# Kernel optimization log

Hardware: AMD Instinct MI355X
Metric: run time of the kernel (lower is better)

The kernel has to match this reference:

```python
import jax, jax.numpy as jnp
import numpy as np

S, P = 64, 32          # scenes, pedestrians per scene (uniform)
N = S * P              # total pedestrians = 2048
H, E = 64, 64          # h_dim, embedding_dim
D1, D2 = 512, 1024     # mlp_pre_pool hidden, bottleneck_dim
EPS = 1e-5             # torch BatchNorm1d eps


def _batchnorm(x, gamma, beta):
    # Training-mode BN with per-scene batch stats (matches the per-scene
    # loop in the original, where BN sees one scene's num_ped^2 rows).
    # x: [S, P*P, D]
    mu = jnp.mean(x, axis=1, keepdims=True)
    var = jnp.mean(jnp.square(x - mu), axis=1, keepdims=True)  # biased var, as torch BN
    return (x - mu) * jax.lax.rsqrt(var + EPS) * gamma + beta


def setup_inputs() -> dict:
    key = jax.random.key(0)
    ks = jax.random.split(key, 16)
    h_states = jax.random.normal(ks[0], (1, N, H), jnp.float32)
    starts = jnp.arange(S, dtype=jnp.int32) * P
    seq_start_end = jnp.stack([starts, starts + P], axis=1)  # [S, 2]
    end_pos = jax.random.normal(ks[1], (N, 2), jnp.float32)
    rel_pos = jax.random.normal(ks[2], (N, 2), jnp.float32)  # unused (pooling_dim=2) but a fwd arg
    sc = 0.05
    params = dict(
        W_embed=jax.random.normal(ks[3], (2, E), jnp.float32) * sc,
        b_embed=jnp.zeros((E,), jnp.float32),
        W1=jax.random.normal(ks[4], (E + H, D1), jnp.float32) * sc,
        b1=jnp.zeros((D1,), jnp.float32),
        g1=jnp.ones((D1,), jnp.float32),
        be1=jnp.zeros((D1,), jnp.float32),
        W2=jax.random.normal(ks[5], (D1, D2), jnp.float32) * sc,
        b2=jnp.zeros((D2,), jnp.float32),
        g2=jnp.ones((D2,), jnp.float32),
        be2=jnp.zeros((D2,), jnp.float32),
    )
    return dict(h_states=h_states, seq_start_end=seq_start_end,
                end_pos=end_pos, rel_pos=rel_pos, **params)


def reference(h_states, seq_start_end, end_pos, rel_pos,
              W_embed, b_embed, W1, b1, g1, be1, W2, b2, g2, be2):
    # Uniform scenes: seq_start_end delimits S contiguous blocks of P peds.
    pos = end_pos.reshape(S, P, 2)
    h = h_states.reshape(N, H).reshape(S, P, H)
    # Original indexing: row (k*P + j) -> pos[j] - pos[k], hidden[j];
    # the final view(P, P, -1).max(1) maxes over j for each k.
    rel = pos[:, None, :, :] - pos[:, :, None, :]          # [S, Pk, Pj, 2]
    emb = rel @ W_embed + b_embed                          # [S, Pk, Pj, E]
    hid = jnp.broadcast_to(h[:, None, :, :], (S, P, P, H)) # hidden of j
    x = jnp.concatenate([emb, hid], axis=-1).reshape(S, P * P, E + H)
    x = jax.nn.relu(_batchnorm(x @ W1 + b1, g1, be1))      # [S, P*P, 512]
    x = jax.nn.relu(_batchnorm(x @ W2 + b2, g2, be2))      # [S, P*P, 1024]
    pool_h = x.reshape(S, P, P, D2).max(axis=2)            # max over j
    return pool_h.reshape(N, D2)
```

## Files before the change

### kernel.cpp

```cpp
#include <hip/hip_runtime.h>
#include <hip/hip_bf16.h>

#define S_ 64
#define P_ 32
#define N_ 2048
#define H_ 64
#define E_ 64
#define D1_ 512
#define D2_ 1024
#define EPS_ 1e-5f

typedef unsigned short u16;
using bf16x8 = __attribute__((ext_vector_type(8))) __bf16;
using floatx4 = __attribute__((ext_vector_type(4))) float;

__device__ inline u16 f2bf(float x) {
    unsigned u = __float_as_uint(x);
    unsigned r = (u + 0x7fffu + ((u >> 16) & 1u)) >> 16;
    return (u16)r;
}


__device__ void prep_scene_256(int u, int tid, float* smem,
                               const float* __restrict__ pos, const float* __restrict__ h,
                               const float* __restrict__ We, const float* __restrict__ W1,
                               const float* __restrict__ g1, const float* __restrict__ be1,
                               float* __restrict__ A, float* __restrict__ Bv) {
    const int s = u >> 2, dq = u & 3;
    const int jg = tid >> 7, dl = tid & 127;
    const int d = (dq << 7) + dl;
    float* hs = smem;
    float* ps = smem + 2048;
    float* red = smem + 2112;
    for (int i = tid; i < 2048; i += 256) hs[i] = h[(size_t)s * 2048 + i];
    if (tid < 64) ps[tid] = pos[s * 64 + tid];
    __syncthreads();
    float wq0 = 0.f, wq1 = 0.f;
    for (int e = 0; e < 64; ++e) {
        const float wv = W1[e * 512 + d];
        wq0 += We[e] * wv;
        wq1 += We[64 + e] * wv;
    }
    float w[16], uu[16];
#pragma unroll
    for (int jj = 0; jj < 16; ++jj) w[jj] = 0.f;
    const float4* h4 = (const float4*)hs;
    for (int e4 = 0; e4 < 16; ++e4) {
        const float c0 = W1[(64 + e4 * 4 + 0) * 512 + d];
        const float c1 = W1[(64 + e4 * 4 + 1) * 512 + d];
        const float c2 = W1[(64 + e4 * 4 + 2) * 512 + d];
        const float c3 = W1[(64 + e4 * 4 + 3) * 512 + d];
#pragma unroll
        for (int jj = 0; jj < 16; ++jj) {
            const float4 hv = h4[((jg << 4) + jj) * 16 + e4];
            w[jj] += hv.x * c0 + hv.y * c1 + hv.z * c2 + hv.w * c3;
        }
    }
    float sw = 0.f, sww = 0.f, su = 0.f, suu = 0.f;
#pragma unroll
    for (int jj = 0; jj < 16; ++jj) {
        const int j = (jg << 4) + jj;
        uu[jj] = ps[2 * j] * wq0 + ps[2 * j + 1] * wq1;
        w[jj] += uu[jj];
        sw += w[jj]; sww += w[jj] * w[jj];
        su += uu[jj]; suu += uu[jj] * uu[jj];
    }
    red[(jg << 7) + dl] = sw;
    red[256 + (jg << 7) + dl] = sww;
    red[512 + (jg << 7) + dl] = su;
    red[768 + (jg << 7) + dl] = suu;
    __syncthreads();
    const float tw = red[dl] + red[128 + dl];
    const float tww = red[256 + dl] + red[384 + dl];
    const float tu = red[512 + dl] + red[640 + dl];
    const float tuu = red[768 + dl] + red[896 + dl];
    const float mw = tw * (1.f / 32.f), mu2 = tu * (1.f / 32.f);
    const float var = (tww * (1.f / 32.f) - mw * mw) + (tuu * (1.f / 32.f) - mu2 * mu2);
    const float sc = rsqrtf(var + EPS_) * g1[d];
    const float bb = be1[d];
#pragma unroll
    for (int jj = 0; jj < 16; ++jj) {
        const int j = (jg << 4) + jj;
        A[(size_t)(s * 32 + j) * 512 + d] = (w[jj] - mw) * sc + bb;
        Bv[(size_t)(s * 32 + j) * 512 + d] = (uu[jj] - mu2) * sc;
    }
}

__device__ void w2t_tile_256(int b2, int tid, void* smem,
                             const float* __restrict__ W2, u16* __restrict__ w2t) {
    float (*tile)[65] = (float (*)[65])smem;
    const int bi = b2 & 15, bj = b2 >> 4;
    const int tx = tid & 63, ty = tid >> 6;
#pragma unroll
    for (int i = 0; i < 64; i += 4)
        tile[ty + i][tx] = W2[(size_t)(bj * 64 + ty + i) * 1024 + bi * 64 + tx];
    __syncthreads();
#pragma unroll
    for (int i = 0; i < 64; i += 4)
        w2t[(size_t)(bi * 64 + ty + i) * 512 + bj * 64 + tx] = f2bf(tile[tx][ty + i]);
}

__global__ __launch_bounds__(256, 2)
void k_gemm(const float* __restrict__ A, const float* __restrict__ Bv,
            const u16* __restrict__ w2t, const float* __restrict__ g2,
            float* __restrict__ ext,
            float* __restrict__ psum, float* __restrict__ psumsq) {
    __shared__ __align__(16) u16 As[128 * 64];
    __shared__ __align__(16) u16 Ws[256 * 64];
    const int tid = threadIdx.x;
    const int bid = blockIdx.x;
    if (bid & 1) {
        __builtin_amdgcn_s_sleep(27);
    }
    const int wave = tid >> 6, lane = tid & 63;
    const int wm = wave >> 1, wn = wave & 1;
    const int quad = lane >> 4, l16 = lane & 15;
    const int lrow = lane >> 3, lchk = lane & 7;
    const int gchk = lchk ^ lrow;
    const int sj = tid >> 3, sc8 = tid & 7;
    const int mt = bid >> 2, cs = bid & 3;
    const int s2 = mt >> 3, rb = mt & 7;
    const int pedb = rb << 2;
    const int N0 = cs << 8;
    const float* Aj = A + ((size_t)(s2 * 32 + sj) << 9) + (sc8 << 3);
    const float* Bp = Bv + ((size_t)(s2 * 32 + pedb) << 9) + (sc8 << 3);
    const int swz = (sc8 ^ (sj & 7)) << 3;

    floatx4 acc[4][8] = {};
    for (int it = 0; it < 8; ++it) {
        const int k0 = it << 6;
#pragma unroll
        for (int t = 0; t < 8; ++t) {
            const int rbase = (wave << 6) + (t << 3);
            const u16* gb = w2t + (size_t)(N0 + rbase + lrow) * 512 + (k0 + (gchk << 3));
            __builtin_amdgcn_global_load_lds(
                (const __attribute__((address_space(1))) void*)gb,
                (__attribute__((address_space(3))) void*)(Ws + (rbase << 6)), 16, 0, 0);
        }
        {
            const float4 alo = *(const float4*)(Aj + k0);
            const float4 ahi = *(const float4*)(Aj + k0 + 4);
#pragma unroll
            for (int p = 0; p < 4; ++p) {
                const int r = (p << 5) + sj;
                const float4 blo = *(const float4*)(Bp + ((size_t)p << 9) + k0);
                const float4 bhi = *(const float4*)(Bp + ((size_t)p << 9) + k0 + 4);
                bf16x8 o;
                o[0] = (__bf16)fmaxf(alo.x - blo.x, 0.f);
                o[1] = (__bf16)fmaxf(alo.y - blo.y, 0.f);
                o[2] = (__bf16)fmaxf(alo.z - blo.z, 0.f);
                o[3] = (__bf16)fmaxf(alo.w - blo.w, 0.f);
                o[4] = (__bf16)fmaxf(ahi.x - bhi.x, 0.f);
                o[5] = (__bf16)fmaxf(ahi.y - bhi.y, 0.f);
                o[6] = (__bf16)fmaxf(ahi.z - bhi.z, 0.f);
                o[7] = (__bf16)fmaxf(ahi.w - bhi.w, 0.f);
                *(bf16x8*)(As + (r << 6) + swz) = o;
            }
        }
        __syncthreads();
#pragma unroll
        for (int kk = 0; kk < 2; ++kk) {
            const int ck = (kk << 2) + quad;
            const int po = (ck ^ (l16 & 7)) << 3;
            bf16x8 af[4], wf[8];
#pragma unroll
            for (int tm = 0; tm < 4; ++tm) {
                const int row = (wm << 6) + (tm << 4) + l16;
                af[tm] = *(const bf16x8*)(As + (row << 6) + po);
            }
#pragma unroll
            for (int tn = 0; tn < 8; ++tn) {
                const int wrow = (wn << 7) + (tn << 4) + l16;
                wf[tn] = *(const bf16x8*)(Ws + (wrow << 6) + ((ck ^ (wrow & 7)) << 3));
            }
#pragma unroll
            for (int tm = 0; tm < 4; ++tm)
#pragma unroll
                for (int tn = 0; tn < 8; ++tn)
                    acc[tm][tn] = __builtin_amdgcn_mfma_f32_16x16x32_bf16(
                        af[tm], wf[tn], acc[tm][tn], 0, 0, 0);
        }
        __syncthreads();
    }
#pragma unroll
    for (int tn = 0; tn < 8; ++tn) {
        const int col = N0 + (wn << 7) + (tn << 4) + l16;
        const float g2v = g2[col];
        float wsum = 0.f, wsq = 0.f;
#pragma unroll
        for (int gp = 0; gp < 2; ++gp) {
            float vmax = -3.4e38f, vmin = 3.4e38f, vs = 0.f, vq = 0.f;
#pragma unroll
            for (int tm = gp * 2; tm < gp * 2 + 2; ++tm)
#pragma unroll
                for (int r = 0; r < 4; ++r) {
                    const float v = acc[tm][tn][r];
                    vmax = fmaxf(vmax, v);
                    vmin = fminf(vmin, v);
                    vs += v;
                    vq += v * v;
                }
#pragma unroll
            for (int off = 16; off < 64; off <<= 1) {
                vmax = fmaxf(vmax, __shfl_xor(vmax, off));
                vmin = fminf(vmin, __shfl_xor(vmin, off));
                vs += __shfl_xor(vs, off);
                vq += __shfl_xor(vq, off);
            }
            if (quad == 0) {
                const int kg = s2 * 32 + pedb + (wm << 1) + gp;
                ext[(size_t)kg * 1024 + col] = (g2v >= 0.f) ? vmax : vmin;
            }
            wsum += vs;
            wsq += vq;
        }
        if (quad == 0) {
            const int slot = (s2 << 4) + (rb << 1) + wm;
            psum[(size_t)slot * 1024 + col] = wsum;
            psumsq[(size_t)slot * 1024 + col] = wsq;
        }
    }
}

__global__ __launch_bounds__(256)
void k_prep(const float* __restrict__ pos, const float* __restrict__ h,
            const float* __restrict__ We, const float* __restrict__ W1,
            const float* __restrict__ g1, const float* __restrict__ be1,
            const float* __restrict__ W2,
            float* __restrict__ A, float* __restrict__ Bv, u16* __restrict__ w2t) {
    __shared__ __align__(16) char smem_raw[16912];
    const int bid = blockIdx.x;
    if (bid < 256)
        prep_scene_256(bid, threadIdx.x, (float*)smem_raw, pos, h, We, W1, g1, be1, A, Bv);
    else
        w2t_tile_256(bid - 256, threadIdx.x, smem_raw, W2, w2t);
}

__global__ __launch_bounds__(256)
void k_final(const float* __restrict__ ext,
             const float* __restrict__ psum, const float* __restrict__ psumsq,
             const float* __restrict__ g2, const float* __restrict__ be2,
             float* __restrict__ out) {
    const int u = blockIdx.x, tid = threadIdx.x;
    const int s3 = u >> 2;
    const int c = ((u & 3) << 8) + tid;
    float sm = 0.f, sq = 0.f;
#pragma unroll
    for (int t = 0; t < 16; ++t) {
        sm += psum[(size_t)(s3 * 16 + t) * 1024 + c];
        sq += psumsq[(size_t)(s3 * 16 + t) * 1024 + c];
    }
    const float mu = sm * (1.f / 1024.f);
    const float var = sq * (1.f / 1024.f) - mu * mu;
    const float inv = rsqrtf(var + EPS_);
    const float scale = g2[c] * inv;
    const float bb = be2[c];
    for (int k = 0; k < 32; ++k) {
        const float v = ext[(size_t)(s3 * 32 + k) * 1024 + c];
        out[(size_t)(s3 * 32 + k) * 1024 + c] = fmaxf((v - mu) * scale + bb, 0.f);
    }
}

extern "C" void kernel_launch(void* const* d_in, const int* in_sizes, int n_in,
                              void* d_out, int out_size, void* d_ws, size_t ws_size,
                              hipStream_t stream) {
    const float* h_states = (const float*)d_in[0];
    const float* end_pos = (const float*)d_in[2];
    const float* W_embed = (const float*)d_in[4];
    const float* W1 = (const float*)d_in[6];
    const float* g1 = (const float*)d_in[8];
    const float* be1 = (const float*)d_in[9];
    const float* W2 = (const float*)d_in[10];
    const float* g2 = (const float*)d_in[12];
    const float* be2 = (const float*)d_in[13];
    float* out = (float*)d_out;

    float* Abuf = (float*)d_ws;
    float* Bbuf = Abuf + 1048576;
    float* ext = Bbuf + 1048576;
    float* psum = ext + 2097152;
    float* psumsq = psum + 1048576;
    u16* w2t = (u16*)(psumsq + 1048576);

    k_prep<<<dim3(384), dim3(256), 0, stream>>>(end_pos, h_states, W_embed, W1,
                                                g1, be1, W2, Abuf, Bbuf, w2t);
    k_gemm<<<dim3(2048), dim3(256), 0, stream>>>(Abuf, Bbuf, w2t, g2,
                                                 ext, psum, psumsq);
    k_final<<<dim3(256), dim3(256), 0, stream>>>(ext, psum, psumsq, g2, be2, out);
}
```

Measured before the change: 180.7 us.

## Fuse BN2 finalize into GEMM with per-scene blocks and in-block stats reduction

Restructures the GEMM grid so each block processes one full scene for a 128-column slice, looping over four 8-pedestrian chunks and accumulating BN sums in registers. The per-scene mean/variance is then reduced in shared memory and the normalize+ReLU output is written in the same kernel, removing the separate finalize kernel and the psum/psumsq workspace traffic. In exchange the grid shrinks fourfold, the block-stagger sleep is dropped, and the epilogue serializes after the GEMM within each block.

Result: slower. 231.0 us (+27.9%).

```diff
diff --git a/kernel.cpp b/kernel.cpp
--- a/kernel.cpp
+++ b/kernel.cpp
@@ -103,121 +103,141 @@
 __global__ __launch_bounds__(256, 2)
 void k_gemm(const float* __restrict__ A, const float* __restrict__ Bv,
             const u16* __restrict__ w2t, const float* __restrict__ g2,
-            float* __restrict__ ext,
-            float* __restrict__ psum, float* __restrict__ psumsq) {
-    __shared__ __align__(16) u16 As[128 * 64];
-    __shared__ __align__(16) u16 Ws[256 * 64];
+            const float* __restrict__ be2,
+            float* __restrict__ ext, float* __restrict__ out) {
+    __shared__ __align__(16) u16 As[256 * 64];
+    __shared__ __align__(16) u16 Ws[128 * 64];
+    __shared__ float red_s[4][128];
+    __shared__ float red_q[4][128];
     const int tid = threadIdx.x;
-    const int bid = blockIdx.x;
-    if (bid & 1) {
-        __builtin_amdgcn_s_sleep(27);
-    }
     const int wave = tid >> 6, lane = tid & 63;
-    const int wm = wave >> 1, wn = wave & 1;
     const int quad = lane >> 4, l16 = lane & 15;
     const int lrow = lane >> 3, lchk = lane & 7;
     const int gchk = lchk ^ lrow;
     const int sj = tid >> 3, sc8 = tid & 7;
-    const int mt = bid >> 2, cs = bid & 3;
-    const int s2 = mt >> 3, rb = mt & 7;
-    const int pedb = rb << 2;
-    const int N0 = cs << 8;
-    const float* Aj = A + ((size_t)(s2 * 32 + sj) << 9) + (sc8 << 3);
-    const float* Bp = Bv + ((size_t)(s2 * 32 + pedb) << 9) + (sc8 << 3);
+    const int bid = blockIdx.x;
+    const int s = bid >> 3, cs = bid & 7;
+    const int N0 = cs << 7;
+    const float* Aj = A + ((size_t)(s * 32 + sj) << 9) + (sc8 << 3);
     const int swz = (sc8 ^ (sj & 7)) << 3;
 
-    floatx4 acc[4][8] = {};
-    for (int it = 0; it < 8; ++it) {
-        const int k0 = it << 6;
-#pragma unroll
-        for (int t = 0; t < 8; ++t) {
-            const int rbase = (wave << 6) + (t << 3);
-            const u16* gb = w2t + (size_t)(N0 + rbase + lrow) * 512 + (k0 + (gchk << 3));
-            __builtin_amdgcn_global_load_lds(
-                (const __attribute__((address_space(1))) void*)gb,
-                (__attribute__((address_space(3))) void*)(Ws + (rbase << 6)), 16, 0, 0);
-        }
-        {
-            const float4 alo = *(const float4*)(Aj + k0);
-            const float4 ahi = *(const float4*)(Aj + k0 + 4);
-#pragma unroll
-            for (int p = 0; p < 4; ++p) {
-                const int r = (p << 5) + sj;
-                const float4 blo = *(const float4*)(Bp + ((size_t)p << 9) + k0);
-                const float4 bhi = *(const float4*)(Bp + ((size_t)p << 9) + k0 + 4);
-                bf16x8 o;
-                o[0] = (__bf16)fmaxf(alo.x - blo.x, 0.f);
-                o[1] = (__bf16)fmaxf(alo.y - blo.y, 0.f);
-                o[2] = (__bf16)fmaxf(alo.z - blo.z, 0.f);
-                o[3] = (__bf16)fmaxf(alo.w - blo.w, 0.f);
-                o[4] = (__bf16)fmaxf(ahi.x - bhi.x, 0.f);
-                o[5] = (__bf16)fmaxf(ahi.y - bhi.y, 0.f);
-                o[6] = (__bf16)fmaxf(ahi.z - bhi.z, 0.f);
-                o[7] = (__bf16)fmaxf(ahi.w - bhi.w, 0.f);
-                *(bf16x8*)(As + (r << 6) + swz) = o;
-            }
-        }
-        __syncthreads();
-#pragma unroll
-        for (int kk = 0; kk < 2; ++kk) {
-            const int ck = (kk << 2) + quad;
-            const int po = (ck ^ (l16 & 7)) << 3;
-            bf16x8 af[4], wf[8];
-#pragma unroll
-            for (int tm = 0; tm < 4; ++tm) {
-                const int row = (wm << 6) + (tm << 4) + l16;
-                af[tm] = *(const bf16x8*)(As + (row << 6) + po);
-            }
-#pragma unroll
-            for (int tn = 0; tn < 8; ++tn) {
-                const int wrow = (wn << 7) + (tn << 4) + l16;
-                wf[tn] = *(const bf16x8*)(Ws + (wrow << 6) + ((ck ^ (wrow & 7)) << 3));
-            }
-#pragma unroll
-            for (int tm = 0; tm < 4; ++tm)
-#pragma unroll
-                for (int tn = 0; tn < 8; ++tn)
-                    acc[tm][tn] = __builtin_amdgcn_mfma_f32_16x16x32_bf16(
-                        af[tm], wf[tn], acc[tm][tn], 0, 0, 0);
-        }
-        __syncthreads();
-    }
-#pragma unroll
-    for (int tn = 0; tn < 8; ++tn) {
-        const int col = N0 + (wn << 7) + (tn << 4) + l16;
-        const float g2v = g2[col];
-        float wsum = 0.f, wsq = 0.f;
-#pragma unroll
-        for (int gp = 0; gp < 2; ++gp) {
-            float vmax = -3.4e38f, vmin = 3.4e38f, vs = 0.f, vq = 0.f;
-#pragma unroll
-            for (int tm = gp * 2; tm < gp * 2 + 2; ++tm)
-#pragma unroll
-                for (int r = 0; r < 4; ++r) {
-                    const float v = acc[tm][tn][r];
-                    vmax = fmaxf(vmax, v);
-                    vmin = fminf(vmin, v);
-                    vs += v;
-                    vq += v * v;
-                }
-#pragma unroll
-            for (int off = 16; off < 64; off <<= 1) {
-                vmax = fmaxf(vmax, __shfl_xor(vmax, off));
-                vmin = fminf(vmin, __shfl_xor(vmin, off));
-                vs += __shfl_xor(vs, off);
-                vq += __shfl_xor(vq, off);
-            }
-            if (quad == 0) {
-                const int kg = s2 * 32 + pedb + (wm << 1) + gp;
-                ext[(size_t)kg * 1024 + col] = (g2v >= 0.f) ? vmax : vmin;
-            }
-            wsum += vs;
-            wsq += vq;
-        }
-        if (quad == 0) {
-            const int slot = (s2 << 4) + (rb << 1) + wm;
-            psum[(size_t)slot * 1024 + col] = wsum;
-            psumsq[(size_t)slot * 1024 + col] = wsq;
+    float wsum_t[8] = {}, wsq_t[8] = {};
+
+    for (int c = 0; c < 4; ++c) {
+        const float* Bp = Bv + ((size_t)(s * 32 + c * 8) << 9) + (sc8 << 3);
+        floatx4 acc[4][8] = {};
+        for (int it = 0; it < 8; ++it) {
+            const int k0 = it << 6;
+#pragma unroll
+            for (int t = 0; t < 4; ++t) {
+                const int rbase = (wave << 5) + (t << 3);
+                const u16* gb = w2t + (size_t)(N0 + rbase + lrow) * 512 + (k0 + (gchk << 3));
+                __builtin_amdgcn_global_load_lds(
+                    (const __attribute__((address_space(1))) void*)gb,
+                    (__attribute__((address_space(3))) void*)(Ws + (rbase << 6)), 16, 0, 0);
+            }
+            {
+                const float4 alo = *(const float4*)(Aj + k0);
+                const float4 ahi = *(const float4*)(Aj + k0 + 4);
+#pragma unroll
+                for (int p = 0; p < 8; ++p) {
+                    const int r = (p << 5) + sj;
+                    const float4 blo = *(const float4*)(Bp + ((size_t)p << 9) + k0);
+                    const float4 bhi = *(const float4*)(Bp + ((size_t)p << 9) + k0 + 4);
+                    bf16x8 o;
+                    o[0] = (__bf16)fmaxf(alo.x - blo.x, 0.f);
+                    o[1] = (__bf16)fmaxf(alo.y - blo.y, 0.f);
+                    o[2] = (__bf16)fmaxf(alo.z - blo.z, 0.f);
+                    o[3] = (__bf16)fmaxf(alo.w - blo.w, 0.f);
+                    o[4] = (__bf16)fmaxf(ahi.x - bhi.x, 0.f);
+                    o[5] = (__bf16)fmaxf(ahi.y - bhi.y, 0.f);
+                    o[6] = (__bf16)fmaxf(ahi.z - bhi.z, 0.f);
+                    o[7] = (__bf16)fmaxf(ahi.w - bhi.w, 0.f);
+                    *(bf16x8*)(As + (r << 6) + swz) = o;
+                }
+            }
+            __syncthreads();
+#pragma unroll
+            for (int kk = 0; kk < 2; ++kk) {
+                const int ck = (kk << 2) + quad;
+                const int po = (ck ^ (l16 & 7)) << 3;
+                bf16x8 af[4], wf[8];
+#pragma unroll
+                for (int tm = 0; tm < 4; ++tm) {
+                    const int row = (wave << 6) + (tm << 4) + l16;
+                    af[tm] = *(const bf16x8*)(As + (row << 6) + po);
+                }
+#pragma unroll
+                for (int tn = 0; tn < 8; ++tn) {
+                    const int wrow = (tn << 4) + l16;
+                    wf[tn] = *(const bf16x8*)(Ws + (wrow << 6) + ((ck ^ (wrow & 7)) << 3));
+                }
+#pragma unroll
+                for (int tm = 0; tm < 4; ++tm)
+#pragma unroll
+                    for (int tn = 0; tn < 8; ++tn)
+                        acc[tm][tn] = __builtin_amdgcn_mfma_f32_16x16x32_bf16(
+                            af[tm], wf[tn], acc[tm][tn], 0, 0, 0);
+            }
+            __syncthreads();
+        }
+#pragma unroll
+        for (int tn = 0; tn < 8; ++tn) {
+            const int colb = (tn << 4) + l16;
+            const float g2v = g2[N0 + colb];
+#pragma unroll
+            for (int gp = 0; gp < 2; ++gp) {
+                float vmax = -3.4e38f, vmin = 3.4e38f, vs = 0.f, vq = 0.f;
+#pragma unroll
+                for (int tm = gp * 2; tm < gp * 2 + 2; ++tm)
+#pragma unroll
+                    for (int r = 0; r < 4; ++r) {
+                        const float v = acc[tm][tn][r];
+                        vmax = fmaxf(vmax, v);
+                        vmin = fminf(vmin, v);
+                        vs += v;
+                        vq += v * v;
+                    }
+#pragma unroll
+                for (int off = 16; off < 64; off <<= 1) {
+                    vmax = fmaxf(vmax, __shfl_xor(vmax, off));
+                    vmin = fminf(vmin, __shfl_xor(vmin, off));
+                    vs += __shfl_xor(vs, off);
+                    vq += __shfl_xor(vq, off);
+                }
+                if (quad == 0) {
+                    const int kg = s * 32 + c * 8 + wave * 2 + gp;
+                    ext[(size_t)kg * 1024 + N0 + colb] = (g2v >= 0.f) ? vmax : vmin;
+                }
+                wsum_t[tn] += vs;
+                wsq_t[tn] += vq;
+            }
+        }
+    }
+
+    if (quad == 0) {
+#pragma unroll
+        for (int tn = 0; tn < 8; ++tn) {
+            red_s[wave][(tn << 4) + l16] = wsum_t[tn];
+            red_q[wave][(tn << 4) + l16] = wsq_t[tn];
+        }
+    }
+    __threadfence_block();
+    __syncthreads();
+    {
+        const int colb = tid & 127, kh = tid >> 7;
+        const float sm = red_s[0][colb] + red_s[1][colb] + red_s[2][colb] + red_s[3][colb];
+        const float sq = red_q[0][colb] + red_q[1][colb] + red_q[2][colb] + red_q[3][colb];
+        const float mu = sm * (1.f / 1024.f);
+        const float var = sq * (1.f / 1024.f) - mu * mu;
+        const float scale = g2[N0 + colb] * rsqrtf(var + EPS_);
+        const float bb = be2[N0 + colb];
+#pragma unroll
+        for (int kq = 0; kq < 16; ++kq) {
+            const int k = (kh << 4) + kq;
+            const float v = ext[(size_t)(s * 32 + k) * 1024 + N0 + colb];
+            out[(size_t)(s * 32 + k) * 1024 + N0 + colb] =
+                fmaxf((v - mu) * scale + bb, 0.f);
         }
     }
 }
@@ -234,31 +254,6 @@
         prep_scene_256(bid, threadIdx.x, (float*)smem_raw, pos, h, We, W1, g1, be1, A, Bv);
     else
         w2t_tile_256(bid - 256, threadIdx.x, smem_raw, W2, w2t);
-}
-
-__global__ __launch_bounds__(256)
-void k_final(const float* __restrict__ ext,
-             const float* __restrict__ psum, const float* __restrict__ psumsq,
-             const float* __restrict__ g2, const float* __restrict__ be2,
-             float* __restrict__ out) {
-    const int u = blockIdx.x, tid = threadIdx.x;
-    const int s3 = u >> 2;
-    const int c = ((u & 3) << 8) + tid;
-    float sm = 0.f, sq = 0.f;
-#pragma unroll
-    for (int t = 0; t < 16; ++t) {
-        sm += psum[(size_t)(s3 * 16 + t) * 1024 + c];
-        sq += psumsq[(size_t)(s3 * 16 + t) * 1024 + c];
-    }
-    const float mu = sm * (1.f / 1024.f);
-    const float var = sq * (1.f / 1024.f) - mu * mu;
-    const float inv = rsqrtf(var + EPS_);
-    const float scale = g2[c] * inv;
-    const float bb = be2[c];
-    for (int k = 0; k < 32; ++k) {
-        const float v = ext[(size_t)(s3 * 32 + k) * 1024 + c];
-        out[(size_t)(s3 * 32 + k) * 1024 + c] = fmaxf((v - mu) * scale + bb, 0.f);
-    }
 }
 
 extern "C" void kernel_launch(void* const* d_in, const int* in_sizes, int n_in,
@@ -278,13 +273,9 @@
     float* Abuf = (float*)d_ws;
     float* Bbuf = Abuf + 1048576;
     float* ext = Bbuf + 1048576;
-    float* psum = ext + 2097152;
-    float* psumsq = psum + 1048576;
-    u16* w2t = (u16*)(psumsq + 1048576);
+    u16* w2t = (u16*)(ext + 2097152);
 
     k_prep<<<dim3(384), dim3(256), 0, stream>>>(end_pos, h_states, W_embed, W1,
                                                 g1, be1, W2, Abuf, Bbuf, w2t);
-    k_gemm<<<dim3(2048), dim3(256), 0, stream>>>(Abuf, Bbuf, w2t, g2,
-                                                 ext, psum, psumsq);
-    k_final<<<dim3(256), dim3(256), 0, stream>>>(ext, psum, psumsq, g2, be2, out);
-}
+    k_gemm<<<dim3(512), dim3(256), 0, stream>>>(Abuf, Bbuf, w2t, g2, be2, ext, out);
+}
```

## Prefetch next K-slice of A/B operands into registers and hand-tune waitcnts

Applied to the files above, without the earlier changes.

Software-pipelines the GEMM main loop. The fp32 A/B operand loads for the next K-slice are issued into registers while the current slice's bf16 tile is built and the MFMAs run. Explicit vmcnt/lgkmcnt waits and raw s_barrier calls replace __syncthreads, so the W2 global_load_lds can complete without draining the prefetch loads. The s_sleep stagger on odd blocks is also removed. This adds about 40 live VGPRs on top of the 128 accumulator registers, and the hand-counted vmcnt(10) has to match the exact number of prefetch loads.

After: 190.6 us. 5.5% more time.

```diff
diff --git a/kernel.cpp b/kernel.cpp
--- a/kernel.cpp
+++ b/kernel.cpp
@@ -100,6 +100,11 @@
         w2t[(size_t)(bi * 64 + ty + i) * 512 + bj * 64 + tx] = f2bf(tile[tx][ty + i]);
 }
 
+#define LGKM0() asm volatile("s_waitcnt lgkmcnt(0)" ::: "memory")
+#define VMC10() asm volatile("s_waitcnt vmcnt(10)" ::: "memory")
+#define VM0()   asm volatile("s_waitcnt vmcnt(0)" ::: "memory")
+#define SCHED_FENCE() __builtin_amdgcn_sched_barrier(0)
+
 __global__ __launch_bounds__(256, 2)
 void k_gemm(const float* __restrict__ A, const float* __restrict__ Bv,
             const u16* __restrict__ w2t, const float* __restrict__ g2,
@@ -109,9 +114,6 @@
     __shared__ __align__(16) u16 Ws[256 * 64];
     const int tid = threadIdx.x;
     const int bid = blockIdx.x;
-    if (bid & 1) {
-        __builtin_amdgcn_s_sleep(27);
-    }
     const int wave = tid >> 6, lane = tid & 63;
     const int wm = wave >> 1, wn = wave & 1;
     const int quad = lane >> 4, l16 = lane & 15;
@@ -126,9 +128,44 @@
     const float* Bp = Bv + ((size_t)(s2 * 32 + pedb) << 9) + (sc8 << 3);
     const int swz = (sc8 ^ (sj & 7)) << 3;
 
+    float4 ra0, ra1, rb0[4], rb1[4];
     floatx4 acc[4][8] = {};
+
+#define LOADR(KX)                                                              \
+    do {                                                                       \
+        ra0 = *(const float4*)(Aj + (KX));                                     \
+        ra1 = *(const float4*)(Aj + (KX) + 4);                                 \
+        _Pragma("unroll")                                                      \
+        for (int p = 0; p < 4; ++p) {                                          \
+            rb0[p] = *(const float4*)(Bp + ((size_t)p << 9) + (KX));           \
+            rb1[p] = *(const float4*)(Bp + ((size_t)p << 9) + (KX) + 4);       \
+        }                                                                      \
+    } while (0)
+
+#define BUILDA()                                                               \
+    do {                                                                       \
+        _Pragma("unroll")                                                      \
+        for (int p = 0; p < 4; ++p) {                                          \
+            const int r = (p << 5) + sj;                                       \
+            bf16x8 o;                                                          \
+            o[0] = (__bf16)fmaxf(ra0.x - rb0[p].x, 0.f);                       \
+            o[1] = (__bf16)fmaxf(ra0.y - rb0[p].y, 0.f);                       \
+            o[2] = (__bf16)fmaxf(ra0.z - rb0[p].z, 0.f);                       \
+            o[3] = (__bf16)fmaxf(ra0.w - rb0[p].w, 0.f);                       \
+            o[4] = (__bf16)fmaxf(ra1.x - rb1[p].x, 0.f);                       \
+            o[5] = (__bf16)fmaxf(ra1.y - rb1[p].y, 0.f);                       \
+            o[6] = (__bf16)fmaxf(ra1.z - rb1[p].z, 0.f);                       \
+            o[7] = (__bf16)fmaxf(ra1.w - rb1[p].w, 0.f);                       \
+            *(bf16x8*)(As + (r << 6) + swz) = o;                               \
+        }                                                                      \
+    } while (0)
+
+    LOADR(0);
+
     for (int it = 0; it < 8; ++it) {
         const int k0 = it << 6;
+        SCHED_FENCE();
+        BUILDA();
 #pragma unroll
         for (int t = 0; t < 8; ++t) {
             const int rbase = (wave << 6) + (t << 3);
@@ -137,27 +174,16 @@
                 (const __attribute__((address_space(1))) void*)gb,
                 (__attribute__((address_space(3))) void*)(Ws + (rbase << 6)), 16, 0, 0);
         }
-        {
-            const float4 alo = *(const float4*)(Aj + k0);
-            const float4 ahi = *(const float4*)(Aj + k0 + 4);
-#pragma unroll
-            for (int p = 0; p < 4; ++p) {
-                const int r = (p << 5) + sj;
-                const float4 blo = *(const float4*)(Bp + ((size_t)p << 9) + k0);
-                const float4 bhi = *(const float4*)(Bp + ((size_t)p << 9) + k0 + 4);
-                bf16x8 o;
-                o[0] = (__bf16)fmaxf(alo.x - blo.x, 0.f);
-                o[1] = (__bf16)fmaxf(alo.y - blo.y, 0.f);
-                o[2] = (__bf16)fmaxf(alo.z - blo.z, 0.f);
-                o[3] = (__bf16)fmaxf(alo.w - blo.w, 0.f);
-                o[4] = (__bf16)fmaxf(ahi.x - bhi.x, 0.f);
-                o[5] = (__bf16)fmaxf(ahi.y - bhi.y, 0.f);
-                o[6] = (__bf16)fmaxf(ahi.z - bhi.z, 0.f);
-                o[7] = (__bf16)fmaxf(ahi.w - bhi.w, 0.f);
-                *(bf16x8*)(As + (r << 6) + swz) = o;
-            }
-        }
-        __syncthreads();
+        SCHED_FENCE();
+        if (it < 7) {
+            LOADR(k0 + 64);
+            VMC10();
+        } else {
+            VM0();
+        }
+        LGKM0();
+        __builtin_amdgcn_s_barrier();
+        SCHED_FENCE();
 #pragma unroll
         for (int kk = 0; kk < 2; ++kk) {
             const int ck = (kk << 2) + quad;
@@ -180,8 +206,11 @@
                     acc[tm][tn] = __builtin_amdgcn_mfma_f32_16x16x32_bf16(
                         af[tm], wf[tn], acc[tm][tn], 0, 0, 0);
         }
-        __syncthreads();
-    }
+        __builtin_amdgcn_s_barrier();
+    }
+#undef LOADR
+#undef BUILDA
+
 #pragma unroll
     for (int tn = 0; tn < 8; ++tn) {
         const int col = N0 + (wn << 7) + (tn << 4) + l16;
```
